# Kernel optimization log

Measured on AMD Instinct MI355X. Metric: run time of the kernel, lower is better.

The kernel has to match this reference:

```python
import jax, jax.numpy as jnp
import numpy as np

B, S, F, U = 64, 512, 128, 512          # seq_length == units (required for broadcast in original code)
SIGDIM = F + F * F                       # level-2 truncated signature dimension
GRID_SIZE, SPLINE_ORDER = 5, 3           # efficient-KAN style defaults
NB = GRID_SIZE + SPLINE_ORDER            # number of b-spline basis functions per input feature
LN_EPS = 1e-3                            # keras LayerNormalization default epsilon


def _make_grid():
    h = 2.0 / GRID_SIZE  # uniform grid on [-1, 1], extended by spline order
    return -1.0 + h * jnp.arange(-SPLINE_ORDER, GRID_SIZE + SPLINE_ORDER + 1, dtype=jnp.float32)


def _b_splines(x, grid):
    # x: (N, F) -> (N, F, NB) via Cox-de Boor recursion
    x = x[..., None]
    bases = ((x >= grid[:-1]) & (x < grid[1:])).astype(x.dtype)
    for p in range(1, SPLINE_ORDER + 1):
        left = (x - grid[:-(p + 1)]) / (grid[p:-1] - grid[:-(p + 1)])
        right = (grid[p + 1:] - x) / (grid[p + 1:] - grid[1:-p])
        bases = left * bases[..., :-1] + right * bases[..., 1:]
    return bases


def _kan_linear(x, base_w, spline_w, grid):
    # KANLinear, no bias / no layernorm: silu base branch + b-spline branch
    lead = x.shape[:-1]
    base = jax.nn.silu(x) @ base_w                                  # (..., U)
    b = _b_splines(x.reshape(-1, x.shape[-1]), grid)                # (N, F, NB)
    spl = jnp.einsum('nfk,ufk->nu', b, spline_w).reshape(*lead, base_w.shape[1])
    return base + spl


def _signature2(x):
    # level-2 path signature of piecewise-linear path x: (B, S, F) -> (B, F + F*F)
    dx = x[:, 1:] - x[:, :-1]                                       # (B, S-1, F)
    s1 = dx.sum(axis=1)                                             # (B, F)
    cs = jnp.cumsum(dx, axis=1)
    prev = jnp.concatenate([jnp.zeros_like(cs[:, :1]), cs[:, :-1]], axis=1)
    s2 = jnp.einsum('bti,btj->bij', prev + 0.5 * dx, dx)            # (B, F, F)
    return jnp.concatenate([s1, s2.reshape(x.shape[0], -1)], axis=-1)


def _grkan(sig, w1, b1, w2, b2, w3, b3, w4, b4, ws, bs, gamma, beta):
    # gated residual network mapping signature -> softmax attention weights (B, U)
    h = jax.nn.elu(sig @ w1 + b1)
    h = h @ w2 + b2
    glu = jax.nn.sigmoid(h @ w3 + b3) * (h @ w4 + b4)
    y = sig @ ws + bs + glu
    mu = jnp.mean(y, axis=-1, keepdims=True)
    var = jnp.var(y, axis=-1, keepdims=True)
    y = (y - mu) / jnp.sqrt(var + LN_EPS) * gamma + beta
    return jax.nn.softmax(y, axis=-1)


def setup_inputs() -> dict:
    key = jax.random.key(0)
    ks = jax.random.split(key, 24)
    n = lambda k, shp, s=0.02: jax.random.normal(k, shp, dtype=jnp.float32) * s
    inp = {
        'inputs': jax.random.normal(ks[0], (B, S, F), dtype=jnp.float32),
        'h_prev': jax.random.normal(ks[1], (B, U), dtype=jnp.float32),
        'c_prev': jax.random.normal(ks[2], (B, U), dtype=jnp.float32),
        'time_kernel': n(ks[3], (S, 1), 0.1),
        'kan_base_w': n(ks[4], (F, U)),
        'kan_spline_w': n(ks[5], (U, F, NB)),
        'g_w1': n(ks[6], (SIGDIM, U)), 'g_b1': jnp.zeros((U,), jnp.float32),
        'g_w2': n(ks[7], (U, U)), 'g_b2': jnp.zeros((U,), jnp.float32),
        'g_w3': n(ks[8], (U, U)), 'g_b3': jnp.zeros((U,), jnp.float32),
        'g_w4': n(ks[9], (U, U)), 'g_b4': jnp.zeros((U,), jnp.float32),
        'g_skip_w': n(ks[10], (SIGDIM, U)), 'g_skip_b': jnp.zeros((U,), jnp.float32),
        'ln_gamma': jnp.ones((U,), jnp.float32), 'ln_beta': jnp.zeros((U,), jnp.float32),
        'wf': n(ks[11], (2 * U, U)), 'bf': jnp.zeros((U,), jnp.float32),
        'wi': n(ks[12], (2 * U, U)), 'bi': jnp.zeros((U,), jnp.float32),
        'wc': n(ks[13], (2 * U, U)), 'bc': jnp.zeros((U,), jnp.float32),
        'wo': n(ks[14], (2 * U, U)), 'bo': jnp.zeros((U,), jnp.float32),
    }
    return inp


def reference(inputs, h_prev, c_prev, time_kernel, kan_base_w, kan_spline_w,
              g_w1, g_b1, g_w2, g_b2, g_w3, g_b3, g_w4, g_b4, g_skip_w, g_skip_b,
              ln_gamma, ln_beta, wf, bf, wi, bi, wc, bc, wo, bo):
    grid = _make_grid()
    weighted = time_kernel * inputs                                  # (B,S,F)
    sig = _signature2(weighted)                                      # (B,SIGDIM)
    attn = _grkan(sig, g_w1, g_b1, g_w2, g_b2, g_w3, g_b3, g_w4, g_b4,
                  g_skip_w, g_skip_b, ln_gamma, ln_beta)             # (B,S) since U==S
    kan_out = _kan_linear(weighted, kan_base_w, kan_spline_w, grid)  # (B,S,U)
    attended = kan_out * attn[..., None]                             # (B,S,U)
    current = attended.mean(axis=1)                                  # (B,U)
    combined = jnp.concatenate([current, h_prev], axis=-1)           # (B,2U)
    f = jax.nn.sigmoid(combined @ wf + bf)
    i = jax.nn.sigmoid(combined @ wi + bi)
    cand = jnp.tanh(combined @ wc + bc)
    o = jax.nn.sigmoid(combined @ wo + bo)
    c_new = f * c_prev + i * cand
    h_new = o * jnp.tanh(c_new)
    return h_new, c_new
```

## Files before the change

### kernel.cpp

```cpp
#include <hip/hip_runtime.h>
#include <math.h>

#define BB 64
#define SS 512
#define FF 128
#define UU 512
#define SIGDIM (FF + FF*FF)
#define K3 16512
#define KK 1152
#define SIG_KC 43
#define SIG_STEPS 6

typedef __attribute__((ext_vector_type(8))) __bf16 bf16x8;
typedef __attribute__((ext_vector_type(8))) unsigned short u16x8;
typedef __attribute__((ext_vector_type(4))) float f32x4;

__device__ __forceinline__ unsigned short f2bf(float x) {
    unsigned int u = __float_as_uint(x);
    unsigned int r = u + 0x7FFFu + ((u >> 16) & 1u);
    return (unsigned short)(r >> 16);
}

__device__ __forceinline__ float sigmoidf(float x) { return 1.0f / (1.0f + expf(-x)); }

__global__ __launch_bounds__(256) void k_prep(const float* __restrict__ splw,
                                              const float* __restrict__ basew,
                                              const float* __restrict__ h_prev,
                                              const float* __restrict__ w2, const float* __restrict__ w3,
                                              const float* __restrict__ w4, const float* __restrict__ wf,
                                              const float* __restrict__ wi, const float* __restrict__ wc,
                                              const float* __restrict__ wo,
                                              unsigned short* __restrict__ Wt,
                                              unsigned short* __restrict__ comb_b,
                                              unsigned short* __restrict__ W2t,
                                              unsigned short* __restrict__ W3t,
                                              unsigned short* __restrict__ W4t,
                                              unsigned short* __restrict__ Wgt) {
    int z = blockIdx.z;
    int tid = threadIdx.x;
    if (z == 0) {
        int base = (blockIdx.y * 16 + blockIdx.x) * 256 + tid;
        {
            int b = base >> 9, uu = base & 511;
            comb_b[(size_t)b * 1024 + 512 + uu] = f2bf(h_prev[base]);
        }
        for (int idx = base; idx < UU * KK; idx += 128 * 256) {
            int u = idx / KK, c = idx % KK;
            float v = (c < 1024) ? splw[(size_t)u * 1024 + c] : basew[(size_t)(c - 1024) * UU + u];
            Wt[idx] = f2bf(v);
        }
        return;
    }
    int zz = z - 1;
    int Kdim = (zz < 3) ? 512 : 1024;
    int kt = blockIdx.x, ut = blockIdx.y;
    if (kt * 64 >= Kdim) return;
    const float* src;
    unsigned short* dst;
    switch (zz) {
        case 0: src = w2; dst = W2t; break;
        case 1: src = w3; dst = W3t; break;
        case 2: src = w4; dst = W4t; break;
        case 3: src = wf; dst = Wgt; break;
        case 4: src = wi; dst = Wgt + (size_t)512 * 1024; break;
        case 5: src = wc; dst = Wgt + (size_t)1024 * 1024; break;
        default: src = wo; dst = Wgt + (size_t)1536 * 1024; break;
    }
    __shared__ float tile[64][67];
    int k0 = kt * 64, u0 = ut * 64;
#pragma unroll
    for (int p = 0; p < 4; ++p) {
        int e = p * 256 + tid;
        int kk = e >> 4, c4 = (e & 15) * 4;
        const float4 v = *(const float4*)(src + (size_t)(k0 + kk) * UU + u0 + c4);
        tile[kk][c4 + 0] = v.x;
        tile[kk][c4 + 1] = v.y;
        tile[kk][c4 + 2] = v.z;
        tile[kk][c4 + 3] = v.w;
    }
    __syncthreads();
    int kk0 = (tid & 7) * 8;
#pragma unroll
    for (int p = 0; p < 2; ++p) {
        int uu = (tid >> 3) + p * 32;
        u16x8 ov;
#pragma unroll
        for (int j = 0; j < 8; ++j) ov[j] = f2bf(tile[kk0 + j][uu]);
        *(u16x8*)(dst + (size_t)(u0 + uu) * Kdim + k0 + kk0) = ov;
    }
}

__global__ __launch_bounds__(256) void k_adprep(const float* __restrict__ inp,
                                                const float* __restrict__ tk,
                                                unsigned short* __restrict__ aT,
                                                unsigned short* __restrict__ dT,
                                                unsigned short* __restrict__ wT) {
    int tt0 = blockIdx.x * 64, f0 = blockIdx.y * 64, b = blockIdx.z;
    __shared__ float wS[65][67];
    __shared__ float w0S[64];
    int tid = threadIdx.x;
    const float* ib = inp + (size_t)b * SS * FF;
    if (tid < 64) w0S[tid] = tk[0] * ib[f0 + tid];
#pragma unroll
    for (int p = 0; p < 5; ++p) {
        int e = p * 256 + tid;
        if (e < 65 * 16) {
            int row = e >> 4, c4 = (e & 15) * 4;
            int t = tt0 + row;
            if (t < SS) {
                float tkt = tk[t];
                const float4 v = *(const float4*)(ib + (size_t)t * FF + f0 + c4);
                wS[row][c4 + 0] = tkt * v.x;
                wS[row][c4 + 1] = tkt * v.y;
                wS[row][c4 + 2] = tkt * v.z;
                wS[row][c4 + 3] = tkt * v.w;
            } else {
                wS[row][c4 + 0] = 0.f;
                wS[row][c4 + 1] = 0.f;
                wS[row][c4 + 2] = 0.f;
                wS[row][c4 + 3] = 0.f;
            }
        }
    }
    __syncthreads();
    int t8 = (tid & 7) * 8;
#pragma unroll
    for (int p = 0; p < 2; ++p) {
        int ff = (tid >> 3) + p * 32;
        float w0 = w0S[ff];
        u16x8 av, dv, wv;
#pragma unroll
        for (int j = 0; j < 8; ++j) {
            int tt = t8 + j;
            float w = wS[tt][ff];
            float wn = wS[tt + 1][ff];
            bool valid = (tt0 + tt) < (SS - 1);
            float a = valid ? 0.5f * (w + wn) - w0 : 0.f;
            float d = valid ? wn - w : 0.f;
            av[j] = f2bf(a);
            dv[j] = f2bf(d);
            wv[j] = f2bf(w);
        }
        size_t o = ((size_t)b * FF + f0 + ff) * SS + tt0 + t8;
        *(u16x8*)(aT + o) = av;
        *(u16x8*)(dT + o) = dv;
        *(u16x8*)(wT + o) = wv;
    }
}

__global__ __launch_bounds__(256) void k_sig_quad(const unsigned short* __restrict__ aT,
                                                  const unsigned short* __restrict__ dT,
                                                  const float* __restrict__ inp,
                                                  const float* __restrict__ tk,
                                                  unsigned short* __restrict__ sigb) {
    int q = blockIdx.x, b = blockIdx.y;
    int qr = q & 1, qc = q >> 1;
    __shared__ unsigned short aS[64][72];
    __shared__ unsigned short dS[64][72];
    int tid = threadIdx.x, lane = tid & 63;
    int wv = __builtin_amdgcn_readfirstlane(tid >> 6);
    int rowoff = (wv & 1) * 32, coloff = (wv >> 1) * 32;
    const unsigned short* pabase = aT + ((size_t)b * FF + qr * 64) * SS;
    const unsigned short* pdbase = dT + ((size_t)b * FF + qc * 64) * SS;

    f32x4 acc[2][2];
#pragma unroll
    for (int i = 0; i < 2; ++i)
#pragma unroll
        for (int j = 0; j < 2; ++j) acc[i][j] = (f32x4)(0.f);

    int arow0 = rowoff + (lane & 15);
    int drow0 = coloff + (lane & 15);
    int kq = (lane >> 4) * 8;

    for (int kc = 0; kc < 8; ++kc) {
#pragma unroll
        for (int p = 0; p < 2; ++p) {
            int e = p * 256 + tid;
            int row = e >> 3, k8 = (e & 7) * 8;
            *(u16x8*)&aS[row][k8] = *(const u16x8*)(pabase + (size_t)row * SS + kc * 64 + k8);
            *(u16x8*)&dS[row][k8] = *(const u16x8*)(pdbase + (size_t)row * SS + kc * 64 + k8);
        }
        __syncthreads();
#pragma unroll
        for (int ks = 0; ks < 2; ++ks) {
            bf16x8 af0 = *(const bf16x8*)&aS[arow0][ks * 32 + kq];
            bf16x8 af1 = *(const bf16x8*)&aS[arow0 + 16][ks * 32 + kq];
            bf16x8 df0 = *(const bf16x8*)&dS[drow0][ks * 32 + kq];
            bf16x8 df1 = *(const bf16x8*)&dS[drow0 + 16][ks * 32 + kq];
            acc[0][0] = __builtin_amdgcn_mfma_f32_16x16x32_bf16(af0, df0, acc[0][0], 0, 0, 0);
            acc[0][1] = __builtin_amdgcn_mfma_f32_16x16x32_bf16(af0, df1, acc[0][1], 0, 0, 0);
            acc[1][0] = __builtin_amdgcn_mfma_f32_16x16x32_bf16(af1, df0, acc[1][0], 0, 0, 0);
            acc[1][1] = __builtin_amdgcn_mfma_f32_16x16x32_bf16(af1, df1, acc[1][1], 0, 0, 0);
        }
        __syncthreads();
    }

    unsigned short* ob = sigb + (size_t)b * SIGDIM;
    if (q == 0 && tid < FF) {
        float v = tk[SS - 1] * inp[((size_t)b * SS + SS - 1) * FF + tid] - tk[0] * inp[(size_t)b * SS * FF + tid];
        ob[tid] = f2bf(v);
    }
    int quad = lane >> 4, col = lane & 15;
#pragma unroll
    for (int rt = 0; rt < 2; ++rt)
#pragma unroll
        for (int ct = 0; ct < 2; ++ct)
#pragma unroll
            for (int reg = 0; reg < 4; ++reg)
                ob[FF + (qr * 64 + rowoff + rt * 16 + quad * 4 + reg) * FF
                      + qc * 64 + coloff + ct * 16 + col] = f2bf(acc[rt][ct][reg]);
}

__global__ __launch_bounds__(256) void k_sig_fused(const unsigned short* __restrict__ sigb,
                                                   const float* __restrict__ w1,
                                                   const float* __restrict__ gsw,
                                                   float* __restrict__ spart) {
    int nt = blockIdx.x, kc = blockIdx.y, mat = blockIdx.z;
    const float* src = mat ? gsw : w1;
    __shared__ float tile[64][67];
    int tid = threadIdx.x, lane = tid & 63;
    int wv = __builtin_amdgcn_readfirstlane(tid >> 6);
    int u0 = nt * 64;
    int n0 = wv * 16;
    int kbase = kc * (SIG_STEPS * 64);

    f32x4 acc[4];
#pragma unroll
    for (int i = 0; i < 4; ++i) acc[i] = (f32x4)(0.f);

    int nn = lane & 15;
    int kq = (lane >> 4) * 8;
    const unsigned short* pab = sigb + (size_t)nn * K3 + kq;

    for (int step = 0; step < SIG_STEPS; ++step) {
        int k0 = kbase + step * 64;
#pragma unroll
        for (int p = 0; p < 4; ++p) {
            int e = p * 256 + tid;
            int kk = e >> 4, c4 = (e & 15) * 4;
            const float4 v = *(const float4*)(src + (size_t)(k0 + kk) * UU + u0 + c4);
            tile[kk][c4 + 0] = v.x;
            tile[kk][c4 + 1] = v.y;
            tile[kk][c4 + 2] = v.z;
            tile[kk][c4 + 3] = v.w;
        }
        __syncthreads();
#pragma unroll
        for (int s = 0; s < 2; ++s) {
            u16x8 ub;
            int kb = s * 32 + kq;
#pragma unroll
            for (int j = 0; j < 8; ++j) ub[j] = f2bf(tile[kb + j][n0 + nn]);
            bf16x8 bfrag = __builtin_bit_cast(bf16x8, ub);
#pragma unroll
            for (int rt = 0; rt < 4; ++rt) {
                bf16x8 afrag = *(const bf16x8*)(pab + (size_t)(rt * 16) * K3 + k0 + s * 32);
                acc[rt] = __builtin_amdgcn_mfma_f32_16x16x32_bf16(afrag, bfrag, acc[rt], 0, 0, 0);
            }
        }
        __syncthreads();
    }

    int col = lane & 15, quad = lane >> 4;
    float* P = spart + ((size_t)(mat * SIG_KC + kc) * 64) * UU;
#pragma unroll
    for (int rt = 0; rt < 4; ++rt)
#pragma unroll
        for (int reg = 0; reg < 4; ++reg)
            P[(size_t)(rt * 16 + quad * 4 + reg) * UU + u0 + n0 + col] = acc[rt][reg];
}

__global__ __launch_bounds__(256) void k_sig_red2(const float* __restrict__ spart,
                                                  const float* __restrict__ b1,
                                                  unsigned short* __restrict__ h1b,
                                                  float* __restrict__ skippre) {
    int idx = blockIdx.x * 256 + threadIdx.x;
    int mat = idx >> 15;
    int rem = idx & 32767;
    int m = rem >> 9, n = rem & 511;
    const float* p = spart + ((size_t)(mat * SIG_KC) * 64 + m) * UU + n;
    float v = 0.f;
#pragma unroll
    for (int kc = 0; kc < SIG_KC; ++kc) v += p[(size_t)kc * 64 * UU];
    if (mat == 0) {
        v += b1[n];
        h1b[(size_t)m * UU + n] = f2bf(v > 0.f ? v : expf(v) - 1.0f);
    } else {
        skippre[(size_t)m * UU + n] = v;
    }
}

__global__ __launch_bounds__(64) void k_grn2(const unsigned short* __restrict__ h1b,
                                             const unsigned short* __restrict__ W2t,
                                             const float* __restrict__ b2,
                                             const unsigned short* __restrict__ W3t,
                                             const unsigned short* __restrict__ W4t,
                                             const float* __restrict__ b3,
                                             const float* __restrict__ b4,
                                             const float* __restrict__ skippre,
                                             const float* __restrict__ skb,
                                             float* __restrict__ yv) {
    int lane = threadIdx.x;
    int mt = blockIdx.x, nt = blockIdx.y;
    __shared__ unsigned short h2S[16][520];
    int col = lane & 15, quad = lane >> 4, kq = quad * 8;

    bf16x8 af[16];
    const unsigned short* pa = h1b + (size_t)(mt * 16 + col) * 512 + kq;
#pragma unroll
    for (int t = 0; t < 16; ++t) af[t] = *(const bf16x8*)(pa + t * 32);

    for (int ct = 0; ct < 32; ++ct) {
        f32x4 acc = (f32x4)(0.f);
        const unsigned short* pb = W2t + (size_t)(ct * 16 + col) * 512 + kq;
#pragma unroll
        for (int t = 0; t < 16; ++t) {
            bf16x8 bf = *(const bf16x8*)(pb + t * 32);
            acc = __builtin_amdgcn_mfma_f32_16x16x32_bf16(af[t], bf, acc, 0, 0, 0);
        }
        float bb = b2[ct * 16 + col];
#pragma unroll
        for (int reg = 0; reg < 4; ++reg)
            h2S[quad * 4 + reg][ct * 16 + col] = f2bf(acc[reg] + bb);
    }
    __syncthreads();

    f32x4 acc3 = (f32x4)(0.f), acc4 = (f32x4)(0.f);
    const unsigned short* pb3 = W3t + (size_t)(nt * 16 + col) * 512 + kq;
    const unsigned short* pb4 = W4t + (size_t)(nt * 16 + col) * 512 + kq;
#pragma unroll
    for (int t = 0; t < 16; ++t) {
        bf16x8 a = *(const bf16x8*)&h2S[col][t * 32 + kq];
        bf16x8 b3f = *(const bf16x8*)(pb3 + t * 32);
        bf16x8 b4f = *(const bf16x8*)(pb4 + t * 32);
        acc3 = __builtin_amdgcn_mfma_f32_16x16x32_bf16(a, b3f, acc3, 0, 0, 0);
        acc4 = __builtin_amdgcn_mfma_f32_16x16x32_bf16(a, b4f, acc4, 0, 0, 0);
    }
    int j = nt * 16 + col;
    float bb3 = b3[j], bb4 = b4[j], sb = skb[j];
#pragma unroll
    for (int reg = 0; reg < 4; ++reg) {
        int row = mt * 16 + quad * 4 + reg;
        float g = sigmoidf(acc3[reg] + bb3);
        yv[(size_t)row * UU + j] = skippre[(size_t)row * UU + j] + sb + g * (acc4[reg] + bb4);
    }
}

__device__ __forceinline__ float block_sum(float v, float* red) {
    int tid = threadIdx.x;
#pragma unroll
    for (int off = 32; off > 0; off >>= 1) v += __shfl_down(v, off);
    __syncthreads();
    if ((tid & 63) == 0) red[tid >> 6] = v;
    __syncthreads();
    float r = red[0];
#pragma unroll
    for (int i = 1; i < 8; ++i) r += red[i];
    return r;
}
__device__ __forceinline__ float block_max(float v, float* red) {
    int tid = threadIdx.x;
#pragma unroll
    for (int off = 32; off > 0; off >>= 1) v = fmaxf(v, __shfl_down(v, off));
    __syncthreads();
    if ((tid & 63) == 0) red[tid >> 6] = v;
    __syncthreads();
    float r = red[0];
#pragma unroll
    for (int i = 1; i < 8; ++i) r = fmaxf(r, red[i]);
    return r;
}

__global__ void k_lnsm(const float* __restrict__ yv, const float* __restrict__ gamma,
                       const float* __restrict__ beta, float* __restrict__ attn) {
    int b = blockIdx.x, u = threadIdx.x;
    __shared__ float red[8];
    float v = yv[(size_t)b * UU + u];
    float mu = block_sum(v, red) * (1.0f / UU);
    float d = v - mu;
    float var = block_sum(d * d, red) * (1.0f / UU);
    float z = d * rsqrtf(var + 1e-3f) * gamma[u] + beta[u];
    float m = block_max(z, red);
    float e = expf(z - m);
    float Z = block_sum(e, red);
    attn[(size_t)b * UU + u] = e / Z;
}

__global__ __launch_bounds__(256) void k_kan_red(const unsigned short* __restrict__ wT,
                                                 const float* __restrict__ attn,
                                                 unsigned short* __restrict__ Aredb) {
    int b = blockIdx.x;
    int lane = threadIdx.x & 63;
    int f = blockIdx.y * 4 + (threadIdx.x >> 6);

    const u16x8 wv = *(const u16x8*)(wT + ((size_t)b * FF + f) * SS + lane * 8);
    const float* ap = attn + (size_t)b * UU + lane * 8;
    float4 a0 = *(const float4*)ap;
    float4 a1 = *(const float4*)(ap + 4);

    float acc[9] = {};
#pragma unroll
    for (int s = 0; s < 8; ++s) {
        float w = __uint_as_float((unsigned int)wv[s] << 16);
        float a = (s < 4) ? ((s == 0) ? a0.x : (s == 1) ? a0.y : (s == 2) ? a0.z : a0.w)
                          : ((s == 4) ? a1.x : (s == 5) ? a1.y : (s == 6) ? a1.z : a1.w);
        float t = (w + 2.2f) * 2.5f;
        float cf = floorf(fminf(fmaxf(t, -2.f), 13.f));
        int c = (int)cf;
        float u = t - cf;
        float u2 = u * u, u3 = u2 * u;
        float p0 = u3 * (1.f / 6.f);
        float p1 = (-3.f * u3 + 3.f * u2 + 3.f * u + 1.f) * (1.f / 6.f);
        float p2 = (3.f * u3 - 6.f * u2 + 4.f) * (1.f / 6.f);
        float onemu = 1.f - u;
        float p3 = onemu * onemu * onemu * (1.f / 6.f);
#pragma unroll
        for (int k2 = 0; k2 < 8; ++k2) {
            int d = c - k2;
            float v = (d == 0) ? p0 : (d == 1) ? p1 : (d == 2) ? p2 : (d == 3) ? p3 : 0.f;
            acc[k2] += a * v;
        }
        acc[8] += a * (w * sigmoidf(w));
    }

#pragma unroll
    for (int off = 1; off < 64; off <<= 1) {
#pragma unroll
        for (int k = 0; k < 9; ++k) acc[k] += __shfl_xor(acc[k], off);
    }

    if (lane == 0) {
        const float sc = 1.0f / SS;
        u16x8 ov;
#pragma unroll
        for (int k = 0; k < 8; ++k) ov[k] = f2bf(acc[k] * sc);
        *(u16x8*)(Aredb + (size_t)b * KK + f * 8) = ov;
        Aredb[(size_t)b * KK + 1024 + f] = f2bf(acc[8] * sc);
    }
}

__global__ __launch_bounds__(64) void k_cur_direct(const unsigned short* __restrict__ Aredb,
                                                   const unsigned short* __restrict__ Wt,
                                                   unsigned short* __restrict__ comb_b) {
    int lane = threadIdx.x;
    int mt = blockIdx.x, nt = blockIdx.y;
    const unsigned short* pa = Aredb + (size_t)(mt * 16 + (lane & 15)) * KK + (lane >> 4) * 8;
    const unsigned short* pb = Wt + (size_t)(nt * 16 + (lane & 15)) * KK + (lane >> 4) * 8;
    f32x4 acc0 = (f32x4)(0.f), acc1 = (f32x4)(0.f);
#pragma unroll 6
    for (int t = 0; t < KK / 32; t += 2) {
        bf16x8 a0 = *(const bf16x8*)(pa + t * 32);
        bf16x8 b0 = *(const bf16x8*)(pb + t * 32);
        bf16x8 a1 = *(const bf16x8*)(pa + t * 32 + 32);
        bf16x8 b1v = *(const bf16x8*)(pb + t * 32 + 32);
        acc0 = __builtin_amdgcn_mfma_f32_16x16x32_bf16(a0, b0, acc0, 0, 0, 0);
        acc1 = __builtin_amdgcn_mfma_f32_16x16x32_bf16(a1, b1v, acc1, 0, 0, 0);
    }
    int col = lane & 15, quad = lane >> 4;
    int j = nt * 16 + col;
#pragma unroll
    for (int reg = 0; reg < 4; ++reg) {
        int row = mt * 16 + quad * 4 + reg;
        comb_b[(size_t)row * 1024 + j] = f2bf(acc0[reg] + acc1[reg]);
    }
}

__global__ __launch_bounds__(64) void k_gates_cell(const unsigned short* __restrict__ comb_b,
                                                   const unsigned short* __restrict__ Wgt,
                                                   const float* __restrict__ bf_,
                                                   const float* __restrict__ bi_,
                                                   const float* __restrict__ bc_,
                                                   const float* __restrict__ bo_,
                                                   const float* __restrict__ c_prev,
                                                   float* __restrict__ out) {
    int lane = threadIdx.x;
    int mt = blockIdx.x, jt = blockIdx.y;
    const unsigned short* pa = comb_b + (size_t)(mt * 16 + (lane & 15)) * 1024 + (lane >> 4) * 8;
    const unsigned short* pb0 = Wgt + (size_t)(0 * 512 + jt * 16 + (lane & 15)) * 1024 + (lane >> 4) * 8;
    const unsigned short* pb1 = Wgt + (size_t)(1 * 512 + jt * 16 + (lane & 15)) * 1024 + (lane >> 4) * 8;
    const unsigned short* pb2 = Wgt + (size_t)(2 * 512 + jt * 16 + (lane & 15)) * 1024 + (lane >> 4) * 8;
    const unsigned short* pb3 = Wgt + (size_t)(3 * 512 + jt * 16 + (lane & 15)) * 1024 + (lane >> 4) * 8;
    f32x4 accf = (f32x4)(0.f), acci = (f32x4)(0.f), accc = (f32x4)(0.f), acco = (f32x4)(0.f);
#pragma unroll 4
    for (int t = 0; t < 32; ++t) {
        bf16x8 a = *(const bf16x8*)(pa + t * 32);
        bf16x8 b0 = *(const bf16x8*)(pb0 + t * 32);
        bf16x8 b1 = *(const bf16x8*)(pb1 + t * 32);
        bf16x8 b2 = *(const bf16x8*)(pb2 + t * 32);
        bf16x8 b3 = *(const bf16x8*)(pb3 + t * 32);
        accf = __builtin_amdgcn_mfma_f32_16x16x32_bf16(a, b0, accf, 0, 0, 0);
        acci = __builtin_amdgcn_mfma_f32_16x16x32_bf16(a, b1, acci, 0, 0, 0);
        accc = __builtin_amdgcn_mfma_f32_16x16x32_bf16(a, b2, accc, 0, 0, 0);
        acco = __builtin_amdgcn_mfma_f32_16x16x32_bf16(a, b3, acco, 0, 0, 0);
    }
    int col = lane & 15, quad = lane >> 4;
    int j = jt * 16 + col;
    float bfv = bf_[j], biv = bi_[j], bcv = bc_[j], bov = bo_[j];
#pragma unroll
    for (int reg = 0; reg < 4; ++reg) {
        int row = mt * 16 + quad * 4 + reg;
        float f = sigmoidf(accf[reg] + bfv);
        float ii = sigmoidf(acci[reg] + biv);
        float cd = tanhf(accc[reg] + bcv);
        float o = sigmoidf(acco[reg] + bov);
        float cn = f * c_prev[(size_t)row * UU + j] + ii * cd;
        out[(size_t)row * UU + j] = o * tanhf(cn);
        out[(size_t)BB * UU + (size_t)row * UU + j] = cn;
    }
}

extern "C" void kernel_launch(void* const* d_in, const int* in_sizes, int n_in,
                              void* d_out, int out_size, void* d_ws, size_t ws_size,
                              hipStream_t stream) {
    const float* inp   = (const float*)d_in[0];
    const float* hprev = (const float*)d_in[1];
    const float* cprev = (const float*)d_in[2];
    const float* tk    = (const float*)d_in[3];
    const float* basew = (const float*)d_in[4];
    const float* splw  = (const float*)d_in[5];
    const float* gw1   = (const float*)d_in[6];
    const float* gb1   = (const float*)d_in[7];
    const float* gw2   = (const float*)d_in[8];
    const float* gb2   = (const float*)d_in[9];
    const float* gw3   = (const float*)d_in[10];
    const float* gb3   = (const float*)d_in[11];
    const float* gw4   = (const float*)d_in[12];
    const float* gb4   = (const float*)d_in[13];
    const float* gsw   = (const float*)d_in[14];
    const float* gsb   = (const float*)d_in[15];
    const float* lng   = (const float*)d_in[16];
    const float* lnb   = (const float*)d_in[17];
    const float* wf    = (const float*)d_in[18];
    const float* bf_   = (const float*)d_in[19];
    const float* wi    = (const float*)d_in[20];
    const float* bi_   = (const float*)d_in[21];
    const float* wc    = (const float*)d_in[22];
    const float* bc_   = (const float*)d_in[23];
    const float* wo    = (const float*)d_in[24];
    const float* bo_   = (const float*)d_in[25];
    float* out = (float*)d_out;

    float* ws = (float*)d_ws;
    size_t o = 0;
    unsigned short* Wt  = (unsigned short*)(ws + o); o += (size_t)UU * KK / 2;
    unsigned short* aT = (unsigned short*)(ws + o); o += (size_t)BB * FF * SS / 2;
    unsigned short* dT = (unsigned short*)(ws + o); o += (size_t)BB * FF * SS / 2;
    unsigned short* wT = (unsigned short*)(ws + o); o += (size_t)BB * FF * SS / 2;
    unsigned short* sigb = (unsigned short*)(ws + o); o += (size_t)BB * K3 / 2;
    float* spart    = ws + o; o += (size_t)2 * SIG_KC * 64 * UU;
    float* skippre  = ws + o; o += (size_t)BB * UU;
    unsigned short* h1b = (unsigned short*)(ws + o); o += (size_t)BB * UU / 2;
    float* yv       = ws + o; o += (size_t)BB * UU;
    float* attn     = ws + o; o += (size_t)BB * UU;
    unsigned short* Aredb = (unsigned short*)(ws + o); o += (size_t)BB * KK / 2;
    unsigned short* W2t = (unsigned short*)(ws + o); o += (size_t)512 * 512 / 2;
    unsigned short* W3t = (unsigned short*)(ws + o); o += (size_t)512 * 512 / 2;
    unsigned short* W4t = (unsigned short*)(ws + o); o += (size_t)512 * 512 / 2;
    unsigned short* Wgt = (unsigned short*)(ws + o); o += (size_t)2048 * 1024 / 2;
    unsigned short* comb_b = (unsigned short*)(ws + o); o += (size_t)BB * 1024 / 2;
    (void)ws_size; (void)in_sizes; (void)n_in; (void)out_size;

    k_prep<<<dim3(16, 8, 8), 256, 0, stream>>>(splw, basew, hprev, gw2, gw3, gw4, wf, wi, wc, wo,
                                               Wt, comb_b, W2t, W3t, W4t, Wgt);
    k_adprep<<<dim3(8, 2, BB), 256, 0, stream>>>(inp, tk, aT, dT, wT);
    k_sig_quad<<<dim3(4, BB), 256, 0, stream>>>(aT, dT, inp, tk, sigb);
    k_sig_fused<<<dim3(8, SIG_KC, 2), 256, 0, stream>>>(sigb, gw1, gsw, spart);
    k_sig_red2<<<256, 256, 0, stream>>>(spart, gb1, h1b, skippre);
    k_grn2<<<dim3(4, 32), 64, 0, stream>>>(h1b, W2t, gb2, W3t, W4t, gb3, gb4, skippre, gsb, yv);
    k_lnsm<<<BB, UU, 0, stream>>>(yv, lng, lnb, attn);
    k_kan_red<<<dim3(BB, FF / 4), 256, 0, stream>>>(wT, attn, Aredb);
    k_cur_direct<<<dim3(4, 32), 64, 0, stream>>>(Aredb, Wt, comb_b);
    k_gates_cell<<<dim3(4, 32), 64, 0, stream>>>(comb_b, Wgt, bf_, bi_, bc_, bo_, cprev, out);
}
```

Measured before the change: 297.8 us.

## Split GRN second stage into separate h2 and GLU kernels removing redundant recompute

The fused GRN kernel had every block recompute the full 16x512 h2 row tile before computing its own 16-column GLU output, duplicating the W2 matmul across all column blocks. The work now runs as two kernels: one computes each h2 tile once and stores it as bf16 in global memory, and the next computes the GLU and skip output reading h2 from global. This trades the redundant MFMA work and W2 traffic for an extra launch and a small global round trip.

```diff
diff --git a/kernel.cpp b/kernel.cpp
--- a/kernel.cpp
+++ b/kernel.cpp
@@ -291,52 +291,57 @@
     }
 }
 
-__global__ __launch_bounds__(64) void k_grn2(const unsigned short* __restrict__ h1b,
-                                             const unsigned short* __restrict__ W2t,
-                                             const float* __restrict__ b2,
-                                             const unsigned short* __restrict__ W3t,
-                                             const unsigned short* __restrict__ W4t,
-                                             const float* __restrict__ b3,
-                                             const float* __restrict__ b4,
-                                             const float* __restrict__ skippre,
-                                             const float* __restrict__ skb,
-                                             float* __restrict__ yv) {
+__global__ __launch_bounds__(64) void k_h2_direct(const unsigned short* __restrict__ h1b,
+                                                  const unsigned short* __restrict__ W2t,
+                                                  const float* __restrict__ b2,
+                                                  unsigned short* __restrict__ h2b) {
     int lane = threadIdx.x;
     int mt = blockIdx.x, nt = blockIdx.y;
-    __shared__ unsigned short h2S[16][520];
-    int col = lane & 15, quad = lane >> 4, kq = quad * 8;
-
-    bf16x8 af[16];
-    const unsigned short* pa = h1b + (size_t)(mt * 16 + col) * 512 + kq;
-#pragma unroll
-    for (int t = 0; t < 16; ++t) af[t] = *(const bf16x8*)(pa + t * 32);
-
-    for (int ct = 0; ct < 32; ++ct) {
-        f32x4 acc = (f32x4)(0.f);
-        const unsigned short* pb = W2t + (size_t)(ct * 16 + col) * 512 + kq;
-#pragma unroll
-        for (int t = 0; t < 16; ++t) {
-            bf16x8 bf = *(const bf16x8*)(pb + t * 32);
-            acc = __builtin_amdgcn_mfma_f32_16x16x32_bf16(af[t], bf, acc, 0, 0, 0);
-        }
-        float bb = b2[ct * 16 + col];
-#pragma unroll
-        for (int reg = 0; reg < 4; ++reg)
-            h2S[quad * 4 + reg][ct * 16 + col] = f2bf(acc[reg] + bb);
-    }
-    __syncthreads();
-
+    const unsigned short* pa = h1b + (size_t)(mt * 16 + (lane & 15)) * 512 + (lane >> 4) * 8;
+    const unsigned short* pb = W2t + (size_t)(nt * 16 + (lane & 15)) * 512 + (lane >> 4) * 8;
+    f32x4 acc0 = (f32x4)(0.f), acc1 = (f32x4)(0.f);
+#pragma unroll
+    for (int t = 0; t < 16; t += 2) {
+        bf16x8 a0 = *(const bf16x8*)(pa + t * 32);
+        bf16x8 b0 = *(const bf16x8*)(pb + t * 32);
+        bf16x8 a1 = *(const bf16x8*)(pa + t * 32 + 32);
+        bf16x8 b1v = *(const bf16x8*)(pb + t * 32 + 32);
+        acc0 = __builtin_amdgcn_mfma_f32_16x16x32_bf16(a0, b0, acc0, 0, 0, 0);
+        acc1 = __builtin_amdgcn_mfma_f32_16x16x32_bf16(a1, b1v, acc1, 0, 0, 0);
+    }
+    int col = lane & 15, quad = lane >> 4;
+    int j = nt * 16 + col;
+    float bb = b2[j];
+#pragma unroll
+    for (int reg = 0; reg < 4; ++reg) {
+        int row = mt * 16 + quad * 4 + reg;
+        h2b[(size_t)row * UU + j] = f2bf(acc0[reg] + acc1[reg] + bb);
+    }
+}
+
+__global__ __launch_bounds__(64) void k_glu_direct(const unsigned short* __restrict__ h2b,
+                                                   const unsigned short* __restrict__ W3t,
+                                                   const unsigned short* __restrict__ W4t,
+                                                   const float* __restrict__ b3,
+                                                   const float* __restrict__ b4,
+                                                   const float* __restrict__ skippre,
+                                                   const float* __restrict__ skb,
+                                                   float* __restrict__ yv) {
+    int lane = threadIdx.x;
+    int mt = blockIdx.x, nt = blockIdx.y;
+    const unsigned short* pa = h2b + (size_t)(mt * 16 + (lane & 15)) * 512 + (lane >> 4) * 8;
+    const unsigned short* pb3 = W3t + (size_t)(nt * 16 + (lane & 15)) * 512 + (lane >> 4) * 8;
+    const unsigned short* pb4 = W4t + (size_t)(nt * 16 + (lane & 15)) * 512 + (lane >> 4) * 8;
     f32x4 acc3 = (f32x4)(0.f), acc4 = (f32x4)(0.f);
-    const unsigned short* pb3 = W3t + (size_t)(nt * 16 + col) * 512 + kq;
-    const unsigned short* pb4 = W4t + (size_t)(nt * 16 + col) * 512 + kq;
 #pragma unroll
     for (int t = 0; t < 16; ++t) {
-        bf16x8 a = *(const bf16x8*)&h2S[col][t * 32 + kq];
+        bf16x8 a = *(const bf16x8*)(pa + t * 32);
         bf16x8 b3f = *(const bf16x8*)(pb3 + t * 32);
         bf16x8 b4f = *(const bf16x8*)(pb4 + t * 32);
         acc3 = __builtin_amdgcn_mfma_f32_16x16x32_bf16(a, b3f, acc3, 0, 0, 0);
         acc4 = __builtin_amdgcn_mfma_f32_16x16x32_bf16(a, b4f, acc4, 0, 0, 0);
     }
+    int col = lane & 15, quad = lane >> 4;
     int j = nt * 16 + col;
     float bb3 = b3[j], bb4 = b4[j], sb = skb[j];
 #pragma unroll
@@ -551,6 +556,7 @@
     float* spart    = ws + o; o += (size_t)2 * SIG_KC * 64 * UU;
     float* skippre  = ws + o; o += (size_t)BB * UU;
     unsigned short* h1b = (unsigned short*)(ws + o); o += (size_t)BB * UU / 2;
+    unsigned short* h2b = (unsigned short*)(ws + o); o += (size_t)BB * UU / 2;
     float* yv       = ws + o; o += (size_t)BB * UU;
     float* attn     = ws + o; o += (size_t)BB * UU;
     unsigned short* Aredb = (unsigned short*)(ws + o); o += (size_t)BB * KK / 2;
@@ -567,7 +573,8 @@
     k_sig_quad<<<dim3(4, BB), 256, 0, stream>>>(aT, dT, inp, tk, sigb);
     k_sig_fused<<<dim3(8, SIG_KC, 2), 256, 0, stream>>>(sigb, gw1, gsw, spart);
     k_sig_red2<<<256, 256, 0, stream>>>(spart, gb1, h1b, skippre);
-    k_grn2<<<dim3(4, 32), 64, 0, stream>>>(h1b, W2t, gb2, W3t, W4t, gb3, gb4, skippre, gsb, yv);
+    k_h2_direct<<<dim3(4, 32), 64, 0, stream>>>(h1b, W2t, gb2, h2b);
+    k_glu_direct<<<dim3(4, 32), 64, 0, stream>>>(h2b, W3t, W4t, gb3, gb4, skippre, gsb, yv);
     k_lnsm<<<BB, UU, 0, stream>>>(yv, lng, lnb, attn);
     k_kan_red<<<dim3(BB, FF / 4), 256, 0, stream>>>(wT, attn, Aredb);
     k_cur_direct<<<dim3(4, 32), 64, 0, stream>>>(Aredb, Wt, comb_b);
```

New measurement: 249.9 us (median of 2 runs). -16.1%, faster.
